# Kernel optimization log

Hardware: AMD Instinct MI355X
Metric: run time of the kernel (lower is better)

## Reference

```python
import jax, jax.numpy as jnp
import numpy as np

N_HEAD = 16


def setup_inputs() -> dict:
    key = jax.random.key(0)
    k1, k2, k3 = jax.random.split(key, 3)
    B, T, C = 2, 2048, 1024
    x = jax.random.normal(k1, (B, T, C), dtype=jnp.float32)
    w_attn = jax.random.normal(k2, (C, 3 * C), dtype=jnp.float32) * 0.02
    w_proj = jax.random.normal(k3, (C, C), dtype=jnp.float32) * 0.02
    return {"x": x, "w_attn": w_attn, "w_proj": w_proj}


def reference(x, w_attn, w_proj):
    B, T, C = x.shape
    H = N_HEAD
    D = C // H
    qkv = x @ w_attn  # [B, T, 3C]
    q, k, v = jnp.split(qkv, 3, axis=2)
    q = q.reshape(B, T, H, D)
    k = k.reshape(B, T, H, D)
    v = v.reshape(B, T, H, D)
    scale = 1.0 / jnp.sqrt(jnp.asarray(D, dtype=x.dtype))
    # Full T x T score matrix, matching the 'standard_attention' path.
    att = jnp.einsum('bthd,bshd->bhts', q, k) * scale  # [B, H, T, T]
    causal = jnp.tril(jnp.ones((T, T), dtype=bool))
    att = jnp.where(causal[None, None, :, :], att, jnp.asarray(-jnp.inf, dtype=att.dtype))
    att = jax.nn.softmax(att, axis=-1)
    # dropout_p is False (== 0.0) in the original module, so no dropout applied.
    y = jnp.einsum('bhts,bshd->bthd', att, v)  # [B, T, H, D]
    y = y.reshape(B, T, C)
    return y @ w_proj
```

## Files before the change

kernel.cpp:

```cpp
#include <hip/hip_runtime.h>
#include <math.h>

#define BB 2
#define TT 2048
#define HH 16
#define DD 64
#define CC 1024
#define C3 3072

typedef __attribute__((ext_vector_type(8))) short bf16x8;
typedef __attribute__((ext_vector_type(4))) short bf16x4;
typedef __attribute__((ext_vector_type(4))) float f32x4;

__device__ __forceinline__ unsigned short f2bf(float f) {
  union { float f; unsigned u; } v; v.f = f;
  unsigned r = v.u + 0x7fffu + ((v.u >> 16) & 1u);
  return (unsigned short)(r >> 16);
}

__device__ __forceinline__ void async_cp16(const void* g, void* l) {
  __builtin_amdgcn_global_load_lds(
      (const __attribute__((address_space(1))) void*)g,
      (__attribute__((address_space(3))) void*)l, 16, 0, 0);
}

__global__ __launch_bounds__(256)
void cvt_bf16(const float* __restrict__ in, unsigned short* __restrict__ out,
              int n4) {
  int i = blockIdx.x * blockDim.x + threadIdx.x;
  const int stride = gridDim.x * blockDim.x;
  for (; i < n4; i += stride) {
    const float4 v = ((const float4*)in)[i];
    bf16x4 o = {(short)f2bf(v.x), (short)f2bf(v.y),
                (short)f2bf(v.z), (short)f2bf(v.w)};
    ((bf16x4*)out)[i] = o;
  }
}

__global__ __launch_bounds__(256)
void transcvt(const float* __restrict__ W, unsigned short* __restrict__ WT,
              int K, int N, float scale_lo, int bound) {
  __shared__ __align__(16) float Ts[64][68];
  const int n0 = blockIdx.x * 64, k0 = blockIdx.y * 64;
  const int rl = threadIdx.x >> 4, c4 = threadIdx.x & 15;
#pragma unroll
  for (int it = 0; it < 4; ++it) {
    const int r = it * 16 + rl;
    *(float4*)&Ts[r][c4 * 4] =
        *(const float4*)(W + (size_t)(k0 + r) * N + n0 + c4 * 4);
  }
  __syncthreads();
#pragma unroll
  for (int it = 0; it < 4; ++it) {
    const int n = it * 16 + rl;
    const float s = (n0 + n < bound) ? scale_lo : 1.0f;
    bf16x4 o = {(short)f2bf(Ts[c4 * 4 + 0][n] * s),
                (short)f2bf(Ts[c4 * 4 + 1][n] * s),
                (short)f2bf(Ts[c4 * 4 + 2][n] * s),
                (short)f2bf(Ts[c4 * 4 + 3][n] * s)};
    *(bf16x4*)(WT + (size_t)(n0 + n) * K + k0 + c4 * 4) = o;
  }
}

constexpr int TK = 32;

template <int OUT_BF16>
__global__ __launch_bounds__(256)
void gemm_bf16(const unsigned short* __restrict__ A,
               const unsigned short* __restrict__ BT,
               void* __restrict__ Cout, int M, int N, int K) {
  __shared__ __align__(16) unsigned short As[128 * TK];
  __shared__ __align__(16) unsigned short Bs[128 * TK];

  const int tid = threadIdx.x;
  const int w = tid >> 6, lane = tid & 63;
  const int l15 = lane & 15, quad = lane >> 4;
  const int wm = w >> 1, wn = w & 1;

  const int row0 = blockIdx.y * 128, col0 = blockIdx.x * 128;

  const int c0 = tid, c1 = tid + 256;
  const int ar0 = c0 >> 2, ak0 = ((c0 & 3) ^ ((c0 >> 3) & 3)) * 8;
  const int ar1 = c1 >> 2, ak1 = ((c1 & 3) ^ ((c1 >> 3) & 3)) * 8;
  const unsigned short* gA0 = A + (size_t)(row0 + ar0) * K + ak0;
  const unsigned short* gA1 = A + (size_t)(row0 + ar1) * K + ak1;
  const unsigned short* gB0 = BT + (size_t)(col0 + ar0) * K + ak0;
  const unsigned short* gB1 = BT + (size_t)(col0 + ar1) * K + ak1;
  const int lds0 = w * 1024, lds1 = 4096 + w * 1024;

  const int fro = l15 * 64 + 16 * (quad ^ ((l15 >> 1) & 3));
  const char* fA = (const char*)As + wm * 4096 + fro;
  const char* fB = (const char*)Bs + wn * 4096 + fro;

  f32x4 acc[4][4];
#pragma unroll
  for (int i = 0; i < 4; ++i)
#pragma unroll
    for (int j = 0; j < 4; ++j) acc[i][j] = (f32x4){0.f, 0.f, 0.f, 0.f};

  for (int k0 = 0; k0 < K; k0 += TK) {
    if (k0) __syncthreads();
    async_cp16(gA0 + k0, (char*)As + lds0);
    async_cp16(gA1 + k0, (char*)As + lds1);
    async_cp16(gB0 + k0, (char*)Bs + lds0);
    async_cp16(gB1 + k0, (char*)Bs + lds1);
    __syncthreads();

    bf16x8 af[4], bf[4];
#pragma unroll
    for (int mt = 0; mt < 4; ++mt) af[mt] = *(const bf16x8*)(fA + mt * 1024);
#pragma unroll
    for (int nt = 0; nt < 4; ++nt) bf[nt] = *(const bf16x8*)(fB + nt * 1024);
#pragma unroll
    for (int mt = 0; mt < 4; ++mt)
#pragma unroll
      for (int nt = 0; nt < 4; ++nt)
        acc[mt][nt] = __builtin_amdgcn_mfma_f32_16x16x32_bf16(
            af[mt], bf[nt], acc[mt][nt], 0, 0, 0);
  }

  if (OUT_BF16) {
    unsigned short* Cb = (unsigned short*)Cout;
#pragma unroll
    for (int mt = 0; mt < 4; ++mt) {
      const int rbase = row0 + wm * 64 + mt * 16 + quad * 4;
#pragma unroll
      for (int r = 0; r < 4; ++r) {
        unsigned short* cr = Cb + (size_t)(rbase + r) * N + col0 + wn * 64 + l15;
#pragma unroll
        for (int nt = 0; nt < 4; ++nt) cr[nt * 16] = f2bf(acc[mt][nt][r]);
      }
    }
  } else {
    float* Cf = (float*)Cout;
#pragma unroll
    for (int mt = 0; mt < 4; ++mt) {
      const int rbase = row0 + wm * 64 + mt * 16 + quad * 4;
#pragma unroll
      for (int r = 0; r < 4; ++r) {
        float* cr = Cf + (size_t)(rbase + r) * N + col0 + wn * 64 + l15;
#pragma unroll
        for (int nt = 0; nt < 4; ++nt) cr[nt * 16] = acc[mt][nt][r];
      }
    }
  }
}

__global__ __launch_bounds__(256)
void vtrans(const unsigned short* __restrict__ qkvb,
            unsigned short* __restrict__ vt) {
  const int t0 = blockIdx.x * 64;
  const int bh = blockIdx.y;
  const int b = bh >> 4, h = bh & 15;
  __shared__ unsigned short Ts[64][68];
  const int tid = threadIdx.x;
  const int rl = tid >> 4, c4 = tid & 15;
  const unsigned short* src = qkvb + (size_t)(b * TT + t0) * C3 + 2048 + h * 64;
#pragma unroll
  for (int it = 0; it < 4; ++it) {
    const int r = it * 16 + rl;
    *(bf16x4*)&Ts[r][c4 * 4] = *(const bf16x4*)(src + (size_t)r * C3 + c4 * 4);
  }
  __syncthreads();
  unsigned short* dst = vt + (size_t)bh * 64 * TT + t0;
#pragma unroll
  for (int it = 0; it < 4; ++it) {
    const int d = it * 16 + rl;
    bf16x4 o = {(short)Ts[c4 * 4 + 0][d], (short)Ts[c4 * 4 + 1][d],
                (short)Ts[c4 * 4 + 2][d], (short)Ts[c4 * 4 + 3][d]};
    *(bf16x4*)(dst + (size_t)d * TT + c4 * 4) = o;
  }
}

__global__ __launch_bounds__(256)
void attn_mfma(const unsigned short* __restrict__ qkvb,
               const unsigned short* __restrict__ vt,
               unsigned short* __restrict__ y) {
  const int qpair = blockIdx.x;
  const int h = blockIdx.y, b = blockIdx.z;
  const int tid = threadIdx.x;
  const int w = tid >> 6;
  const int lane = tid & 63;
  const int l15 = lane & 15, quad = lane >> 4;

  __shared__ __align__(16) char Kb[2 * 8192];
  __shared__ __align__(16) char Vb[2 * 8192];
  __shared__ __align__(16) unsigned short Ps[64 * 76];
  unsigned short* psw = Ps + w * 16 * 76;

  const int lr = lane >> 3;
  const int lc = lane & 7;
  const int srcoff = ((lc ^ lr) << 4);
  const char* ksrc = (const char*)qkvb + ((size_t)(b * TT) * C3 + 1024 + h * 64) * 2;
  const char* vsrc = (const char*)vt + ((size_t)(b * HH + h) * DD * TT) * 2;

  const int fro = l15 * 128 + ((quad ^ (l15 & 7)) << 4);

  for (int phase = 0; phase < 2; ++phase) {
    const int qt = phase == 0 ? 31 - qpair : qpair;

    if (phase) __syncthreads();

    const unsigned short* qrow =
        qkvb + (size_t)(b * TT + qt * 64 + w * 16 + l15) * C3 + h * DD;
    bf16x8 qf0 = *(const bf16x8*)(qrow + quad * 8);
    bf16x8 qf1 = *(const bf16x8*)(qrow + 32 + quad * 8);

    f32x4 O[4];
#pragma unroll
    for (int ct = 0; ct < 4; ++ct) O[ct] = (f32x4){0.f, 0.f, 0.f, 0.f};
    float psum[4] = {0.f, 0.f, 0.f, 0.f};

#pragma unroll
    for (int i = 0; i < 2; ++i) {
      async_cp16(ksrc + (size_t)(w * 16 + i * 8 + lr) * (C3 * 2) + srcoff,
                 Kb + w * 2048 + i * 1024);
      async_cp16(vsrc + (size_t)(w * 16 + i * 8 + lr) * (TT * 2) + srcoff,
                 Vb + w * 2048 + i * 1024);
    }

    for (int j = 0; j <= qt; ++j) {
      const int cur = j & 1;
      __syncthreads();

      if (j < qt) {
        const int key1 = (j + 1) * 64;
        char* kd = Kb + (cur ^ 1) * 8192 + w * 2048;
        char* vd = Vb + (cur ^ 1) * 8192 + w * 2048;
#pragma unroll
        for (int i = 0; i < 2; ++i) {
          async_cp16(
              ksrc + (size_t)(key1 + w * 16 + i * 8 + lr) * (C3 * 2) + srcoff,
              kd + i * 1024);
          async_cp16(
              vsrc + (size_t)(w * 16 + i * 8 + lr) * (TT * 2) + key1 * 2 + srcoff,
              vd + i * 1024);
        }
      }

      const char* Kc = Kb + cur * 8192;
      const char* Vc = Vb + cur * 8192;

      f32x4 S[4];
#pragma unroll
      for (int ct = 0; ct < 4; ++ct) {
        bf16x8 k0 = *(const bf16x8*)(Kc + ct * 2048 + fro);
        bf16x8 k1 = *(const bf16x8*)(Kc + ct * 2048 + (fro ^ 64));
        f32x4 z = {0.f, 0.f, 0.f, 0.f};
        z = __builtin_amdgcn_mfma_f32_16x16x32_bf16(qf0, k0, z, 0, 0, 0);
        z = __builtin_amdgcn_mfma_f32_16x16x32_bf16(qf1, k1, z, 0, 0, 0);
        S[ct] = z;
      }

      if (j == qt) {
#pragma unroll
        for (int ct = 0; ct < 4; ++ct)
#pragma unroll
          for (int r = 0; r < 4; ++r)
            if (16 * ct + l15 > w * 16 + quad * 4 + r) S[ct][r] = -INFINITY;
      }

      float P[4][4];
#pragma unroll
      for (int ct = 0; ct < 4; ++ct)
#pragma unroll
        for (int r = 0; r < 4; ++r) {
          P[ct][r] = exp2f(S[ct][r] - 12.0f);
          psum[r] += P[ct][r];
        }

#pragma unroll
      for (int ct = 0; ct < 4; ++ct)
#pragma unroll
        for (int r = 0; r < 4; ++r)
          psw[(quad * 4 + r) * 76 + 16 * ct + l15] = f2bf(P[ct][r]);

      bf16x8 pf[2];
#pragma unroll
      for (int kh = 0; kh < 2; ++kh) {
        const unsigned short* pr = psw + l15 * 76 + kh * 32 + quad * 8;
        bf16x4 lo = *(const bf16x4*)(pr);
        bf16x4 hi = *(const bf16x4*)(pr + 4);
        bf16x8 f;
#pragma unroll
        for (int jj = 0; jj < 4; ++jj) { f[jj] = lo[jj]; f[4 + jj] = hi[jj]; }
        pf[kh] = f;
      }

#pragma unroll
      for (int ct = 0; ct < 4; ++ct) {
        bf16x8 v0 = *(const bf16x8*)(Vc + ct * 2048 + fro);
        bf16x8 v1 = *(const bf16x8*)(Vc + ct * 2048 + (fro ^ 64));
        O[ct] = __builtin_amdgcn_mfma_f32_16x16x32_bf16(pf[0], v0, O[ct], 0, 0, 0);
        O[ct] = __builtin_amdgcn_mfma_f32_16x16x32_bf16(pf[1], v1, O[ct], 0, 0, 0);
      }
    }

#pragma unroll
    for (int off = 1; off < 16; off <<= 1)
#pragma unroll
      for (int r = 0; r < 4; ++r) psum[r] += __shfl_xor(psum[r], off, 64);

    unsigned short* yr =
        y + (size_t)(b * TT + qt * 64 + w * 16 + quad * 4) * CC + h * DD + l15;
#pragma unroll
    for (int r = 0; r < 4; ++r) {
      const float inv = 1.0f / psum[r];
#pragma unroll
      for (int ct = 0; ct < 4; ++ct)
        yr[(size_t)r * CC + 16 * ct] = f2bf(O[ct][r] * inv);
    }
  }
}

extern "C" void kernel_launch(void* const* d_in, const int* in_sizes, int n_in,
                              void* d_out, int out_size, void* d_ws,
                              size_t ws_size, hipStream_t stream) {
  const float* x      = (const float*)d_in[0];
  const float* w_attn = (const float*)d_in[1];
  const float* w_proj = (const float*)d_in[2];
  float* out = (float*)d_out;

  unsigned short* xb   = (unsigned short*)d_ws;
  unsigned short* wat  = xb + (size_t)4096 * 1024;
  unsigned short* wpt  = wat + (size_t)3072 * 1024;
  unsigned short* qkvb = wpt + (size_t)1024 * 1024;
  unsigned short* vt   = qkvb + (size_t)4096 * 3072;
  unsigned short* yb   = vt + (size_t)BB * HH * DD * TT;

  dim3 blk(256);

  cvt_bf16<<<2048, blk, 0, stream>>>(x, xb, 4096 * 1024 / 4);
  transcvt<<<dim3(C3 / 64, CC / 64), blk, 0, stream>>>(
      w_attn, wat, CC, C3, 0.18033688f , 1024);
  transcvt<<<dim3(CC / 64, CC / 64), blk, 0, stream>>>(
      w_proj, wpt, CC, CC, 1.0f, 0);

  gemm_bf16<1><<<dim3(C3 / 128, (BB * TT) / 128), blk, 0, stream>>>(
      xb, wat, qkvb, BB * TT, C3, CC);

  vtrans<<<dim3(TT / 64, BB * HH), blk, 0, stream>>>(qkvb, vt);

  attn_mfma<<<dim3(16, HH, BB), blk, 0, stream>>>(qkvb, vt, yb);

  gemm_bf16<0><<<dim3(CC / 128, (BB * TT) / 128), blk, 0, stream>>>(
      yb, wpt, out, BB * TT, CC, CC);
}
```

Before: 196.7 us.

## Fuse prep kernels, write V transposed from QKV GEMM, MFMA row-sums in attention

Merges the x conversion and both weight transpose-conversions into one prep launch, and drops the separate vtrans kernel by having the QKV GEMM write the V columns directly in transposed layout. The attention kernel now folds the -12 softmax offset into the MFMA accumulator init and computes row sums with an extra MFMA against a ones vector, replacing the per-element adds and shuffle reductions. It also remaps blocks to a flattened 1D grid, and the output projection uses 64-row tiles so more blocks run. This trades fewer launches and less scalar work for strided transposed V stores and round-half-up bf16 rounding of the probabilities.

New measurement: 189.8 us. 1.04x faster.

```diff
diff --git a/kernel.cpp b/kernel.cpp
--- a/kernel.cpp
+++ b/kernel.cpp
@@ -17,6 +17,10 @@
   unsigned r = v.u + 0x7fffu + ((v.u >> 16) & 1u);
   return (unsigned short)(r >> 16);
 }
+__device__ __forceinline__ unsigned short f2bf_up(float f) {
+  union { float f; unsigned u; } v; v.f = f;
+  return (unsigned short)((v.u + 0x8000u) >> 16);
+}
 
 __device__ __forceinline__ void async_cp16(const void* g, void* l) {
   __builtin_amdgcn_global_load_lds(
@@ -25,59 +29,71 @@
 }
 
 __global__ __launch_bounds__(256)
-void cvt_bf16(const float* __restrict__ in, unsigned short* __restrict__ out,
-              int n4) {
-  int i = blockIdx.x * blockDim.x + threadIdx.x;
-  const int stride = gridDim.x * blockDim.x;
-  for (; i < n4; i += stride) {
-    const float4 v = ((const float4*)in)[i];
-    bf16x4 o = {(short)f2bf(v.x), (short)f2bf(v.y),
-                (short)f2bf(v.z), (short)f2bf(v.w)};
-    ((bf16x4*)out)[i] = o;
-  }
-}
-
-__global__ __launch_bounds__(256)
-void transcvt(const float* __restrict__ W, unsigned short* __restrict__ WT,
-              int K, int N, float scale_lo, int bound) {
+void prep(const float* __restrict__ x, const float* __restrict__ w_attn,
+          const float* __restrict__ w_proj, unsigned short* __restrict__ xb,
+          unsigned short* __restrict__ wat, unsigned short* __restrict__ wpt) {
   __shared__ __align__(16) float Ts[64][68];
-  const int n0 = blockIdx.x * 64, k0 = blockIdx.y * 64;
-  const int rl = threadIdx.x >> 4, c4 = threadIdx.x & 15;
+  const int bx = blockIdx.x, tid = threadIdx.x;
+  if (bx < 1024) {
+    int i = bx * 256 + tid;
+#pragma unroll
+    for (int it = 0; it < 4; ++it, i += 262144) {
+      const float4 v = ((const float4*)x)[i];
+      bf16x4 o = {(short)f2bf(v.x), (short)f2bf(v.y),
+                  (short)f2bf(v.z), (short)f2bf(v.w)};
+      ((bf16x4*)xb)[i] = o;
+    }
+    return;
+  }
+  const float* W;
+  unsigned short* WT;
+  int Nd, bound, n0, k0;
+  float s;
+  if (bx < 1792) {
+    const int bid = bx - 1024;
+    W = w_attn; WT = wat; Nd = 3072; bound = 1024; s = 0.18033688f;
+    n0 = (bid % 48) * 64; k0 = (bid / 48) * 64;
+  } else {
+    const int bid = bx - 1792;
+    W = w_proj; WT = wpt; Nd = 1024; bound = 0; s = 1.0f;
+    n0 = (bid % 16) * 64; k0 = (bid / 16) * 64;
+  }
+  const int rl = tid >> 4, c4 = tid & 15;
 #pragma unroll
   for (int it = 0; it < 4; ++it) {
     const int r = it * 16 + rl;
     *(float4*)&Ts[r][c4 * 4] =
-        *(const float4*)(W + (size_t)(k0 + r) * N + n0 + c4 * 4);
+        *(const float4*)(W + (size_t)(k0 + r) * Nd + n0 + c4 * 4);
   }
   __syncthreads();
 #pragma unroll
   for (int it = 0; it < 4; ++it) {
     const int n = it * 16 + rl;
-    const float s = (n0 + n < bound) ? scale_lo : 1.0f;
-    bf16x4 o = {(short)f2bf(Ts[c4 * 4 + 0][n] * s),
-                (short)f2bf(Ts[c4 * 4 + 1][n] * s),
-                (short)f2bf(Ts[c4 * 4 + 2][n] * s),
-                (short)f2bf(Ts[c4 * 4 + 3][n] * s)};
-    *(bf16x4*)(WT + (size_t)(n0 + n) * K + k0 + c4 * 4) = o;
-  }
-}
-
-constexpr int TK = 32;
-
-template <int OUT_BF16>
+    const float sc = (n0 + n < bound) ? s : 1.0f;
+    bf16x4 o = {(short)f2bf(Ts[c4 * 4 + 0][n] * sc),
+                (short)f2bf(Ts[c4 * 4 + 1][n] * sc),
+                (short)f2bf(Ts[c4 * 4 + 2][n] * sc),
+                (short)f2bf(Ts[c4 * 4 + 3][n] * sc)};
+    *(bf16x4*)(WT + (size_t)(n0 + n) * CC + k0 + c4 * 4) = o;
+  }
+}
+
+template <int MODE, int BM>
 __global__ __launch_bounds__(256)
 void gemm_bf16(const unsigned short* __restrict__ A,
                const unsigned short* __restrict__ BT,
-               void* __restrict__ Cout, int M, int N, int K) {
-  __shared__ __align__(16) unsigned short As[128 * TK];
-  __shared__ __align__(16) unsigned short Bs[128 * TK];
+               void* __restrict__ Cout, unsigned short* __restrict__ Vout,
+               int M, int N, int K) {
+  constexpr int MT = BM / 32;
+  __shared__ __align__(16) unsigned short As[BM * 32];
+  __shared__ __align__(16) unsigned short Bs[128 * 32];
 
   const int tid = threadIdx.x;
   const int w = tid >> 6, lane = tid & 63;
   const int l15 = lane & 15, quad = lane >> 4;
   const int wm = w >> 1, wn = w & 1;
 
-  const int row0 = blockIdx.y * 128, col0 = blockIdx.x * 128;
+  const int row0 = blockIdx.y * BM, col0 = blockIdx.x * 128;
 
   const int c0 = tid, c1 = tid + 256;
   const int ar0 = c0 >> 2, ak0 = ((c0 & 3) ^ ((c0 >> 3) & 3)) * 8;
@@ -89,41 +105,54 @@
   const int lds0 = w * 1024, lds1 = 4096 + w * 1024;
 
   const int fro = l15 * 64 + 16 * (quad ^ ((l15 >> 1) & 3));
-  const char* fA = (const char*)As + wm * 4096 + fro;
+  const char* fA = (const char*)As + wm * (BM * 32) + fro;
   const char* fB = (const char*)Bs + wn * 4096 + fro;
 
-  f32x4 acc[4][4];
-#pragma unroll
-  for (int i = 0; i < 4; ++i)
+  f32x4 acc[MT][4];
+#pragma unroll
+  for (int i = 0; i < MT; ++i)
 #pragma unroll
     for (int j = 0; j < 4; ++j) acc[i][j] = (f32x4){0.f, 0.f, 0.f, 0.f};
 
-  for (int k0 = 0; k0 < K; k0 += TK) {
+  for (int k0 = 0; k0 < K; k0 += 32) {
     if (k0) __syncthreads();
     async_cp16(gA0 + k0, (char*)As + lds0);
-    async_cp16(gA1 + k0, (char*)As + lds1);
+    if (BM == 128) async_cp16(gA1 + k0, (char*)As + lds1);
     async_cp16(gB0 + k0, (char*)Bs + lds0);
     async_cp16(gB1 + k0, (char*)Bs + lds1);
     __syncthreads();
 
-    bf16x8 af[4], bf[4];
-#pragma unroll
-    for (int mt = 0; mt < 4; ++mt) af[mt] = *(const bf16x8*)(fA + mt * 1024);
+    bf16x8 af[MT], bf[4];
+#pragma unroll
+    for (int mt = 0; mt < MT; ++mt) af[mt] = *(const bf16x8*)(fA + mt * 1024);
 #pragma unroll
     for (int nt = 0; nt < 4; ++nt) bf[nt] = *(const bf16x8*)(fB + nt * 1024);
 #pragma unroll
-    for (int mt = 0; mt < 4; ++mt)
+    for (int mt = 0; mt < MT; ++mt)
 #pragma unroll
       for (int nt = 0; nt < 4; ++nt)
         acc[mt][nt] = __builtin_amdgcn_mfma_f32_16x16x32_bf16(
             af[mt], bf[nt], acc[mt][nt], 0, 0, 0);
   }
 
-  if (OUT_BF16) {
+  if (MODE == 2 && col0 >= 2048) {
+#pragma unroll
+    for (int mt = 0; mt < MT; ++mt) {
+      const int rbase = row0 + wm * (BM / 2) + mt * 16 + quad * 4;
+      const int bq = rbase >> 11, t0 = rbase & 2047;
+#pragma unroll
+      for (int nt = 0; nt < 4; ++nt) {
+        const int col = col0 + wn * 64 + nt * 16 + l15;
+        bf16x4 o = {(short)f2bf(acc[mt][nt][0]), (short)f2bf(acc[mt][nt][1]),
+                    (short)f2bf(acc[mt][nt][2]), (short)f2bf(acc[mt][nt][3])};
+        *(bf16x4*)(Vout + ((size_t)((bq << 10) + col - 2048) << 11) + t0) = o;
+      }
+    }
+  } else if (MODE >= 1) {
     unsigned short* Cb = (unsigned short*)Cout;
 #pragma unroll
-    for (int mt = 0; mt < 4; ++mt) {
-      const int rbase = row0 + wm * 64 + mt * 16 + quad * 4;
+    for (int mt = 0; mt < MT; ++mt) {
+      const int rbase = row0 + wm * (BM / 2) + mt * 16 + quad * 4;
 #pragma unroll
       for (int r = 0; r < 4; ++r) {
         unsigned short* cr = Cb + (size_t)(rbase + r) * N + col0 + wn * 64 + l15;
@@ -134,8 +163,8 @@
   } else {
     float* Cf = (float*)Cout;
 #pragma unroll
-    for (int mt = 0; mt < 4; ++mt) {
-      const int rbase = row0 + wm * 64 + mt * 16 + quad * 4;
+    for (int mt = 0; mt < MT; ++mt) {
+      const int rbase = row0 + wm * (BM / 2) + mt * 16 + quad * 4;
 #pragma unroll
       for (int r = 0; r < 4; ++r) {
         float* cr = Cf + (size_t)(rbase + r) * N + col0 + wn * 64 + l15;
@@ -143,32 +172,6 @@
         for (int nt = 0; nt < 4; ++nt) cr[nt * 16] = acc[mt][nt][r];
       }
     }
-  }
-}
-
-__global__ __launch_bounds__(256)
-void vtrans(const unsigned short* __restrict__ qkvb,
-            unsigned short* __restrict__ vt) {
-  const int t0 = blockIdx.x * 64;
-  const int bh = blockIdx.y;
-  const int b = bh >> 4, h = bh & 15;
-  __shared__ unsigned short Ts[64][68];
-  const int tid = threadIdx.x;
-  const int rl = tid >> 4, c4 = tid & 15;
-  const unsigned short* src = qkvb + (size_t)(b * TT + t0) * C3 + 2048 + h * 64;
-#pragma unroll
-  for (int it = 0; it < 4; ++it) {
-    const int r = it * 16 + rl;
-    *(bf16x4*)&Ts[r][c4 * 4] = *(const bf16x4*)(src + (size_t)r * C3 + c4 * 4);
-  }
-  __syncthreads();
-  unsigned short* dst = vt + (size_t)bh * 64 * TT + t0;
-#pragma unroll
-  for (int it = 0; it < 4; ++it) {
-    const int d = it * 16 + rl;
-    bf16x4 o = {(short)Ts[c4 * 4 + 0][d], (short)Ts[c4 * 4 + 1][d],
-                (short)Ts[c4 * 4 + 2][d], (short)Ts[c4 * 4 + 3][d]};
-    *(bf16x4*)(dst + (size_t)d * TT + c4 * 4) = o;
   }
 }
 
@@ -176,8 +179,10 @@
 void attn_mfma(const unsigned short* __restrict__ qkvb,
                const unsigned short* __restrict__ vt,
                unsigned short* __restrict__ y) {
-  const int qpair = blockIdx.x;
-  const int h = blockIdx.y, b = blockIdx.z;
+  const int n = blockIdx.x;
+  const int bh = (n & 7) + 8 * ((n >> 3) & 3);
+  const int qpair = n >> 5;
+  const int b = bh >> 4, h = bh & 15;
   const int tid = threadIdx.x;
   const int w = tid >> 6;
   const int lane = tid & 63;
@@ -196,6 +201,11 @@
 
   const int fro = l15 * 128 + ((quad ^ (l15 & 7)) << 4);
 
+  bf16x8 onesf;
+#pragma unroll
+  for (int jj = 0; jj < 8; ++jj)
+    onesf[jj] = (short)(l15 == 0 ? 0x3F80 : 0);
+
   for (int phase = 0; phase < 2; ++phase) {
     const int qt = phase == 0 ? 31 - qpair : qpair;
 
@@ -209,7 +219,7 @@
     f32x4 O[4];
 #pragma unroll
     for (int ct = 0; ct < 4; ++ct) O[ct] = (f32x4){0.f, 0.f, 0.f, 0.f};
-    float psum[4] = {0.f, 0.f, 0.f, 0.f};
+    f32x4 lacc = (f32x4){0.f, 0.f, 0.f, 0.f};
 
 #pragma unroll
     for (int i = 0; i < 2; ++i) {
@@ -246,7 +256,7 @@
       for (int ct = 0; ct < 4; ++ct) {
         bf16x8 k0 = *(const bf16x8*)(Kc + ct * 2048 + fro);
         bf16x8 k1 = *(const bf16x8*)(Kc + ct * 2048 + (fro ^ 64));
-        f32x4 z = {0.f, 0.f, 0.f, 0.f};
+        f32x4 z = (f32x4){-12.f, -12.f, -12.f, -12.f};
         z = __builtin_amdgcn_mfma_f32_16x16x32_bf16(qf0, k0, z, 0, 0, 0);
         z = __builtin_amdgcn_mfma_f32_16x16x32_bf16(qf1, k1, z, 0, 0, 0);
         S[ct] = z;
@@ -260,20 +270,11 @@
             if (16 * ct + l15 > w * 16 + quad * 4 + r) S[ct][r] = -INFINITY;
       }
 
-      float P[4][4];
 #pragma unroll
       for (int ct = 0; ct < 4; ++ct)
 #pragma unroll
-        for (int r = 0; r < 4; ++r) {
-          P[ct][r] = exp2f(S[ct][r] - 12.0f);
-          psum[r] += P[ct][r];
-        }
-
-#pragma unroll
-      for (int ct = 0; ct < 4; ++ct)
-#pragma unroll
         for (int r = 0; r < 4; ++r)
-          psw[(quad * 4 + r) * 76 + 16 * ct + l15] = f2bf(P[ct][r]);
+          psw[(quad * 4 + r) * 76 + 16 * ct + l15] = f2bf_up(exp2f(S[ct][r]));
 
       bf16x8 pf[2];
 #pragma unroll
@@ -287,6 +288,8 @@
         pf[kh] = f;
       }
 
+      lacc = __builtin_amdgcn_mfma_f32_16x16x32_bf16(pf[0], onesf, lacc, 0, 0, 0);
+      lacc = __builtin_amdgcn_mfma_f32_16x16x32_bf16(pf[1], onesf, lacc, 0, 0, 0);
 #pragma unroll
       for (int ct = 0; ct < 4; ++ct) {
         bf16x8 v0 = *(const bf16x8*)(Vc + ct * 2048 + fro);
@@ -296,20 +299,18 @@
       }
     }
 
-#pragma unroll
-    for (int off = 1; off < 16; off <<= 1)
-#pragma unroll
-      for (int r = 0; r < 4; ++r) psum[r] += __shfl_xor(psum[r], off, 64);
+    float inv[4];
+#pragma unroll
+    for (int r = 0; r < 4; ++r)
+      inv[r] = 1.0f / __shfl(lacc[r], lane & 48, 64);
 
     unsigned short* yr =
         y + (size_t)(b * TT + qt * 64 + w * 16 + quad * 4) * CC + h * DD + l15;
 #pragma unroll
-    for (int r = 0; r < 4; ++r) {
-      const float inv = 1.0f / psum[r];
+    for (int r = 0; r < 4; ++r)
 #pragma unroll
       for (int ct = 0; ct < 4; ++ct)
-        yr[(size_t)r * CC + 16 * ct] = f2bf(O[ct][r] * inv);
-    }
+        yr[(size_t)r * CC + 16 * ct] = f2bf(O[ct][r] * inv[r]);
   }
 }
 
@@ -330,19 +331,13 @@
 
   dim3 blk(256);
 
-  cvt_bf16<<<2048, blk, 0, stream>>>(x, xb, 4096 * 1024 / 4);
-  transcvt<<<dim3(C3 / 64, CC / 64), blk, 0, stream>>>(
-      w_attn, wat, CC, C3, 0.18033688f , 1024);
-  transcvt<<<dim3(CC / 64, CC / 64), blk, 0, stream>>>(
-      w_proj, wpt, CC, CC, 1.0f, 0);
-
-  gemm_bf16<1><<<dim3(C3 / 128, (BB * TT) / 128), blk, 0, stream>>>(
-      xb, wat, qkvb, BB * TT, C3, CC);
-
-  vtrans<<<dim3(TT / 64, BB * HH), blk, 0, stream>>>(qkvb, vt);
-
-  attn_mfma<<<dim3(16, HH, BB), blk, 0, stream>>>(qkvb, vt, yb);
-
-  gemm_bf16<0><<<dim3(CC / 128, (BB * TT) / 128), blk, 0, stream>>>(
-      yb, wpt, out, BB * TT, CC, CC);
-}
+  prep<<<2048, blk, 0, stream>>>(x, w_attn, w_proj, xb, wat, wpt);
+
+  gemm_bf16<2, 128><<<dim3(C3 / 128, (BB * TT) / 128), blk, 0, stream>>>(
+      xb, wat, qkvb, vt, BB * TT, C3, CC);
+
+  attn_mfma<<<dim3(512, 1, 1), blk, 0, stream>>>(qkvb, vt, yb);
+
+  gemm_bf16<0, 64><<<dim3(CC / 128, (BB * TT) / 64), blk, 0, stream>>>(
+      yb, wpt, out, nullptr, BB * TT, CC, CC);
+}
```
